# Performance work log

Measured on AMD Instinct MI355X. Metric: run time of the kernel, lower is better.

## Reference

```python
import jax, jax.numpy as jnp
import numpy as np
from jax import lax

NUM_CLASSES = 2
NUM_PROTO = 10
C = 720


def _conv(x, w, b, pad):
    # x: [B,Cin,H,W], w: [Cout,Cin,kh,kw]
    y = lax.conv_general_dilated(x, w, (1, 1), ((pad, pad), (pad, pad)),
                                 dimension_numbers=('NCHW', 'OIHW', 'NCHW'))
    return y + b[None, :, None, None]


def _bn(x, g, b, rm, rv):
    inv = g / jnp.sqrt(rv + 1e-5)
    return (x - rm[None, :, None, None]) * inv[None, :, None, None] + b[None, :, None, None]


def _ln(x, g, b):
    mu = jnp.mean(x, -1, keepdims=True)
    var = jnp.var(x, -1, keepdims=True)
    return (x - mu) / jnp.sqrt(var + 1e-5) * g + b


def _l2n(x):
    n = jnp.linalg.norm(x, axis=-1, keepdims=True)
    return x / jnp.maximum(n, 1e-12)


def _resize_bilinear_ac(x, oh, ow):
    # bilinear with align_corners=True, x: [B,C,H,W]
    B, Cc, H, W = x.shape
    ys = jnp.linspace(0.0, H - 1.0, oh)
    xs = jnp.linspace(0.0, W - 1.0, ow)
    y0 = jnp.floor(ys).astype(jnp.int32)
    y1 = jnp.minimum(y0 + 1, H - 1)
    wy = (ys - y0).astype(x.dtype)
    x0 = jnp.floor(xs).astype(jnp.int32)
    x1 = jnp.minimum(x0 + 1, W - 1)
    wx = (xs - x0).astype(x.dtype)
    r = x[:, :, y0, :] * (1 - wy)[None, None, :, None] + x[:, :, y1, :] * wy[None, None, :, None]
    return r[:, :, :, x0] * (1 - wx) + r[:, :, :, x1] * wx


def setup_inputs() -> dict:
    key = jax.random.key(0)
    ks = jax.random.split(key, 8)
    B, H = 2, 96
    f32 = jnp.float32
    return {
        'feat1': jax.random.normal(ks[0], (B, 48, H, H), f32),
        'feat2': jax.random.normal(ks[1], (B, 96, H // 2, H // 2), f32),
        'feat3': jax.random.normal(ks[2], (B, 192, H // 4, H // 4), f32),
        'feat4': jax.random.normal(ks[3], (B, 384, H // 8, H // 8), f32),
        'cls_w': jax.random.normal(ks[4], (C, C, 3, 3), f32) * 0.02,
        'cls_b': jnp.zeros((C,), f32),
        'cls_bn_g': jnp.ones((C,), f32),
        'cls_bn_b': jnp.zeros((C,), f32),
        'cls_bn_rm': jnp.zeros((C,), f32),
        'cls_bn_rv': jnp.ones((C,), f32),
        'proj_w1': jax.random.normal(ks[5], (C, C, 1, 1), f32) * 0.02,
        'proj_b1': jnp.zeros((C,), f32),
        'proj_bn_g': jnp.ones((C,), f32),
        'proj_bn_b': jnp.zeros((C,), f32),
        'proj_bn_rm': jnp.zeros((C,), f32),
        'proj_bn_rv': jnp.ones((C,), f32),
        'proj_w2': jax.random.normal(ks[6], (C, C, 1, 1), f32) * 0.02,
        'proj_b2': jnp.zeros((C,), f32),
        'ln_feat_g': jnp.ones((C,), f32),
        'ln_feat_b': jnp.zeros((C,), f32),
        'ln_mask_g': jnp.ones((NUM_CLASSES,), f32),
        'ln_mask_b': jnp.zeros((NUM_CLASSES,), f32),
        'prototypes': jax.random.normal(ks[7], (NUM_CLASSES, NUM_PROTO, C), f32) * 0.02,
    }


def reference(feat1, feat2, feat3, feat4, cls_w, cls_b, cls_bn_g, cls_bn_b, cls_bn_rm,
              cls_bn_rv, proj_w1, proj_b1, proj_bn_g, proj_bn_b, proj_bn_rm, proj_bn_rv,
              proj_w2, proj_b2, ln_feat_g, ln_feat_b, ln_mask_g, ln_mask_b, prototypes):
    B, _, h, w = feat1.shape
    feats = jnp.concatenate([
        feat1,
        _resize_bilinear_ac(feat2, h, w),
        _resize_bilinear_ac(feat3, h, w),
        _resize_bilinear_ac(feat4, h, w),
    ], axis=1)  # [B,720,h,w]
    # cls_head: Conv3x3 + BN + ReLU (Dropout2d is identity in eval)
    c = jax.nn.relu(_bn(_conv(feats, cls_w, cls_b, 1), cls_bn_g, cls_bn_b, cls_bn_rm, cls_bn_rv))
    # proj_head (convmlp): Conv1x1 + BN + ReLU + Conv1x1
    p = jax.nn.relu(_bn(_conv(c, proj_w1, proj_b1, 0), proj_bn_g, proj_bn_b, proj_bn_rm, proj_bn_rv))
    p = _conv(p, proj_w2, proj_b2, 0)
    # (b h w) c
    _c = p.transpose(0, 2, 3, 1).reshape(-1, C)
    _c = _l2n(_ln(_c, ln_feat_g, ln_feat_b))
    protos = _l2n(prototypes)  # [K,M,C]
    masks = jnp.einsum('nd,kmd->nmk', _c, protos)  # [N,M,K]
    out_seg = jnp.max(masks, axis=1)               # [N,K]
    out_seg = _ln(out_seg, ln_mask_g, ln_mask_b)
    out_seg = out_seg.reshape(B, h, w, NUM_CLASSES).transpose(0, 3, 1, 2)
    return out_seg
```

## Files before the change

### kernel.cpp

```cpp
#include <hip/hip_runtime.h>
#include <float.h>

#define WDIM 96
#define HW   9216
#define PH   98
#define IMG  (PH*PH)
#define NPIXP (2*IMG)
#define NPIX 19328
#define GUARD 128
#define GPIX (NPIX + 2*GUARD)
#define NKG_ACT 96
#define MDIM 768
#define G3 816
#define G1 96

typedef _Float16 f16;
typedef f16  f16x8 __attribute__((ext_vector_type(8)));
typedef f16  f16x4 __attribute__((ext_vector_type(4)));
typedef float f32x4 __attribute__((ext_vector_type(4)));

__global__ void prep_kernel(
    const float* __restrict__ cls_b,
    const float* __restrict__ g0, const float* __restrict__ b0,
    const float* __restrict__ rm0, const float* __restrict__ rv0,
    const float* __restrict__ p1b,
    const float* __restrict__ g1, const float* __restrict__ b1,
    const float* __restrict__ rm1, const float* __restrict__ rv1,
    const float* __restrict__ p2b,
    const float* __restrict__ protos,
    float* __restrict__ alpha, float* __restrict__ beta,
    float* __restrict__ protoN)
{
    __shared__ float red[4];
    if (blockIdx.x == 0) {
        for (int i = threadIdx.x; i < MDIM; i += blockDim.x) {
            if (i < 720) {
                float s0 = g0[i] * rsqrtf(rv0[i] + 1e-5f);
                alpha[i] = s0;
                beta[i]  = (cls_b[i] - rm0[i]) * s0 + b0[i];
                float s1 = g1[i] * rsqrtf(rv1[i] + 1e-5f);
                alpha[MDIM + i] = s1;
                beta[MDIM + i]  = (p1b[i] - rm1[i]) * s1 + b1[i];
                alpha[2*MDIM + i] = 1.0f;
                beta[2*MDIM + i]  = p2b[i];
            } else {
                alpha[i] = 0.f; beta[i] = 0.f;
                alpha[MDIM + i] = 0.f; beta[MDIM + i] = 0.f;
                alpha[2*MDIM + i] = 0.f; beta[2*MDIM + i] = 0.f;
            }
        }
    } else {
        int row = blockIdx.x - 1;
        const float* src = protos + row * 720;
        float s = 0.f;
        for (int i = threadIdx.x; i < 720; i += blockDim.x) { float v = src[i]; s += v * v; }
        #pragma unroll
        for (int off = 32; off > 0; off >>= 1) s += __shfl_down(s, off);
        int wave = threadIdx.x >> 6, lane = threadIdx.x & 63;
        if (lane == 0) red[wave] = s;
        __syncthreads();
        float tot = red[0] + red[1] + red[2] + red[3];
        float rn = 1.0f / fmaxf(sqrtf(tot), 1e-12f);
        for (int i = threadIdx.x; i < 720; i += blockDim.x)
            protoN[row * 720 + i] = src[i] * rn;
    }
}

__global__ __launch_bounds__(256)
void w3trans_kernel(const float* __restrict__ w3,
                    f16* __restrict__ W3h, f16* __restrict__ W3l)
{
    int tid = blockIdx.x * blockDim.x + threadIdx.x;
    int kgl = tid / MDIM;
    int o   = tid - kgl * MDIM;
    if (kgl > 90) return;

    if (kgl == 90) {
        f16x8 z = {0, 0, 0, 0, 0, 0, 0, 0};
        for (int g = 810; g < G3; ++g) {
            size_t off = ((size_t)g * MDIM + o) * 8;
            *(f16x8*)(W3h + off) = z;
            *(f16x8*)(W3l + off) = z;
        }
        return;
    }

    float buf[72];
    if (o < 720) {
        const float* src = w3 + (size_t)o * 6480 + kgl * 72;
        #pragma unroll
        for (int c = 0; c < 72; ++c) buf[c] = src[c];
    } else {
        #pragma unroll
        for (int c = 0; c < 72; ++c) buf[c] = 0.f;
    }

    #pragma unroll
    for (int s = 0; s < 9; ++s) {
        f16x8 hv, lv;
        #pragma unroll
        for (int c = 0; c < 8; ++c) {
            float v = buf[c * 9 + s];
            f16 h = (f16)v;
            hv[c] = h;
            lv[c] = (f16)(v - (float)h);
        }
        size_t off = ((size_t)(kgl * 9 + s) * MDIM + o) * 8;
        *(f16x8*)(W3h + off) = hv;
        *(f16x8*)(W3l + off) = lv;
    }
}

__global__ void w1trans_kernel(const float* __restrict__ w1a,
                               const float* __restrict__ w1b,
                               f16* __restrict__ W1ah, f16* __restrict__ W1al,
                               f16* __restrict__ W1bh, f16* __restrict__ W1bl)
{
    int tid = blockIdx.x * blockDim.x + threadIdx.x;
    const int N1 = G1 * MDIM;
    const float* src; f16 *dh, *dl; int g, o;
    if (tid < N1)            { g = tid / MDIM; o = tid - g * MDIM; src = w1a; dh = W1ah; dl = W1al; }
    else if (tid < 2 * N1)   { int u = tid - N1; g = u / MDIM; o = u - g * MDIM; src = w1b; dh = W1bh; dl = W1bl; }
    else return;

    float v[8];
    #pragma unroll
    for (int j = 0; j < 8; ++j) v[j] = 0.f;
    if (g < 90 && o < 720) {
        #pragma unroll
        for (int j = 0; j < 8; ++j)
            v[j] = src[(size_t)o * 720 + g * 8 + j];
    }
    f16x8 hv, lv;
    #pragma unroll
    for (int j = 0; j < 8; ++j) {
        f16 h = (f16)v[j];
        hv[j] = h;
        lv[j] = (f16)(v[j] - (float)h);
    }
    size_t off = ((size_t)g * MDIM + o) * 8;
    *(f16x8*)(dh + off) = hv;
    *(f16x8*)(dl + off) = lv;
}

__global__ void upsample_kernel(const float* __restrict__ f1,
                                const float* __restrict__ f2,
                                const float* __restrict__ f3,
                                const float* __restrict__ f4,
                                f16* __restrict__ Xhi, f16* __restrict__ Xlo)
{
    int tid = blockIdx.x * blockDim.x + threadIdx.x;
    if (tid >= 90 * GPIX) return;
    int kg = tid / GPIX;
    int gp = tid - kg * GPIX;
    int p  = gp - GUARD;
    float v[8];
    #pragma unroll
    for (int j = 0; j < 8; ++j) v[j] = 0.f;
    if (p >= 0 && p < NPIXP) {
        int b = p / IMG; int rem = p - b * IMG;
        int y = rem / PH; int x = rem - y * PH;
        if (y >= 1 && y <= 96 && x >= 1 && x <= 96) {
            int oy = y - 1, ox = x - 1;
            int c0 = kg * 8;
            if (c0 < 48) {
                #pragma unroll
                for (int j = 0; j < 8; ++j)
                    v[j] = f1[((size_t)(b * 48 + c0 + j)) * HW + oy * 96 + ox];
            } else {
                const float* src; int Cs, Hs, cb;
                if (c0 < 144)      { src = f2; Cs = 96;  Hs = 48; cb = c0 - 48; }
                else if (c0 < 336) { src = f3; Cs = 192; Hs = 24; cb = c0 - 144; }
                else               { src = f4; Cs = 384; Hs = 12; cb = c0 - 336; }
                float scale = (float)(Hs - 1) / 95.0f;
                float yf = oy * scale, xf = ox * scale;
                int y0 = (int)yf, x0 = (int)xf;
                float wy = yf - y0, wx = xf - x0;
                int y1 = min(y0 + 1, Hs - 1), x1 = min(x0 + 1, Hs - 1);
                #pragma unroll
                for (int j = 0; j < 8; ++j) {
                    const float* sb = src + (size_t)(b * Cs + cb + j) * Hs * Hs;
                    float v00 = sb[y0 * Hs + x0], v01 = sb[y0 * Hs + x1];
                    float v10 = sb[y1 * Hs + x0], v11 = sb[y1 * Hs + x1];
                    float r0 = v00 * (1.f - wy) + v10 * wy;
                    float r1 = v01 * (1.f - wy) + v11 * wy;
                    v[j] = r0 * (1.f - wx) + r1 * wx;
                }
            }
        }
    }
    f16x8 hv, lv;
    #pragma unroll
    for (int j = 0; j < 8; ++j) {
        f16 h = (f16)v[j];
        hv[j] = h;
        lv[j] = (f16)(v[j] - (float)h);
    }
    size_t off = (size_t)tid * 8;
    *(f16x8*)(Xhi + off) = hv;
    *(f16x8*)(Xlo + off) = lv;
}

template<int NSTEP, int CONV3>
__global__ __launch_bounds__(256, 2)
void mfma_gemm(const f16* __restrict__ Whi, const f16* __restrict__ Wlo,
               const f16* __restrict__ Bhi_, const f16* __restrict__ Blo_,
               f16* __restrict__ Ohi, f16* __restrict__ Olo,
               const float* __restrict__ alpha, const float* __restrict__ beta,
               int relu)
{
    const int l = blockIdx.x;
    const int xcd = l & 7;
    const int j0 = l >> 3;
    const int ncol = xcd * 19 + j0 / 6;
    if (ncol >= 151) return;
    const int m0 = (j0 % 6) * 128;
    const int n0 = ncol * 128;

    const int t = threadIdx.x;
    const int lane = t & 63, wid = t >> 6;
    const int wm = wid >> 1, wn = wid & 1;
    const int quad = lane >> 4, ln = lane & 15;

    f32x4 acc[4][4];
    #pragma unroll
    for (int i = 0; i < 4; ++i)
        #pragma unroll
        for (int j = 0; j < 4; ++j)
            acc[i][j] = (f32x4){0.f, 0.f, 0.f, 0.f};

    const int arow = m0 + wm * 64 + ln;
    const f16* Ah0 = Whi + ((size_t)quad * MDIM + arow) * 8;
    const f16* Al0 = Wlo + ((size_t)quad * MDIM + arow) * 8;
    const size_t astep = (size_t)4 * MDIM * 8;

    const int bcol = n0 + wn * 64 + ln;

    auto brow_of = [&](int step) -> long long {
        const int g = step * 4 + quad;
        if (CONV3) {
            int gc = min(g, 809);
            int kgl = gc / 9;
            int s = gc - kgl * 9;
            int d = (s / 3 - 1) * PH + (s % 3 - 1);
            return (long long)kgl * GPIX + d;
        }
        return (long long)min(g, G1 - 1) * GPIX;
    };

    auto load_b = [&](f16x8 (&dst)[8], int step) {
        const long long brow = brow_of(step);
        const f16* bh = Bhi_ + (brow + bcol) * 8;
        const f16* bl = Blo_ + (brow + bcol) * 8;
        #pragma unroll
        for (int nt = 0; nt < 4; ++nt) {
            dst[nt]     = *(const f16x8*)(bh + nt * 128);
            dst[nt + 4] = *(const f16x8*)(bl + nt * 128);
        }
    };
    auto load_a = [&](f16x8 (&dst)[8], int step) {
        const f16* Ah = Ah0 + (size_t)step * astep;
        const f16* Al = Al0 + (size_t)step * astep;
        #pragma unroll
        for (int mt = 0; mt < 4; ++mt) {
            dst[mt]     = *(const f16x8*)(Ah + mt * 128);
            dst[mt + 4] = *(const f16x8*)(Al + mt * 128);
        }
    };
    auto compute = [&](f16x8 (&av)[8], f16x8 (&bv)[8]) {
        #pragma unroll
        for (int mt = 0; mt < 4; ++mt)
            #pragma unroll
            for (int nt = 0; nt < 4; ++nt) {
                acc[mt][nt] = __builtin_amdgcn_mfma_f32_16x16x32_f16(av[mt],     bv[nt],     acc[mt][nt], 0, 0, 0);
                acc[mt][nt] = __builtin_amdgcn_mfma_f32_16x16x32_f16(av[mt],     bv[nt + 4], acc[mt][nt], 0, 0, 0);
                acc[mt][nt] = __builtin_amdgcn_mfma_f32_16x16x32_f16(av[mt + 4], bv[nt],     acc[mt][nt], 0, 0, 0);
            }
    };

    f16x8 aP[8], bP[8], aQ[8], bQ[8];

    load_a(aP, 0);
    load_b(bP, 0);

    int step = 0;
    #pragma unroll 1
    for (; step + 2 <= NSTEP; step += 2) {
        load_a(aQ, step + 1);
        load_b(bQ, step + 1);
        compute(aP, bP);
        load_a(aP, step + 2);
        load_b(bP, step + 2);
        compute(aQ, bQ);
    }
    if (step < NSTEP)
        compute(aP, bP);

    #pragma unroll
    for (int mt = 0; mt < 4; ++mt) {
        const int rowb = m0 + wm * 64 + mt * 16 + quad * 4;
        const float4 a4 = *(const float4*)(alpha + rowb);
        const float4 b4 = *(const float4*)(beta + rowb);
        const size_t kg = rowb >> 3;
        const int sub = rowb & 7;
        #pragma unroll
        for (int nt = 0; nt < 4; ++nt) {
            const int P = n0 + wn * 64 + nt * 16 + ln;
            float v0 = acc[mt][nt][0] * a4.x + b4.x;
            float v1 = acc[mt][nt][1] * a4.y + b4.y;
            float v2 = acc[mt][nt][2] * a4.z + b4.z;
            float v3 = acc[mt][nt][3] * a4.w + b4.w;
            if (relu) {
                v0 = fmaxf(v0, 0.f); v1 = fmaxf(v1, 0.f);
                v2 = fmaxf(v2, 0.f); v3 = fmaxf(v3, 0.f);
            }
            f16 h0 = (f16)v0, h1 = (f16)v1, h2 = (f16)v2, h3 = (f16)v3;
            f16x4 hv = {h0, h1, h2, h3};
            f16x4 lv = {(f16)(v0 - (float)h0), (f16)(v1 - (float)h1),
                        (f16)(v2 - (float)h2), (f16)(v3 - (float)h3)};
            size_t o = (kg * GPIX + P) * 8 + sub;
            *(f16x4*)(Ohi + o) = hv;
            *(f16x4*)(Olo + o) = lv;
        }
    }
}

__global__ __launch_bounds__(256)
void head_kernel(const f16* __restrict__ Yhi, const f16* __restrict__ Ylo,
                 const float* __restrict__ lng, const float* __restrict__ lnb,
                 const float* __restrict__ protoN,
                 const float* __restrict__ lmg, const float* __restrict__ lmb,
                 float* __restrict__ out)
{
    const int t = threadIdx.x;
    const int wv = t >> 6, lane = t & 63;
    const int pw = lane >> 4, sub = lane & 15;
    const int p = blockIdx.x * 16 + wv * 4 + pw;
    const int b = p / HW; const int r = p - b * HW;
    const int y = r / 96; const int x = r - y * 96;
    const size_t P = (size_t)b * IMG + (y + 1) * PH + (x + 1);

    f16x8 xh[6], xl[6];
    float s1 = 0.f, s2 = 0.f;
    #pragma unroll
    for (int k = 0; k < 6; ++k) {
        int kg = sub + 16 * k;
        if (kg < 90) {
            xh[k] = *(const f16x8*)(Yhi + ((size_t)kg * GPIX + P) * 8);
            xl[k] = *(const f16x8*)(Ylo + ((size_t)kg * GPIX + P) * 8);
            #pragma unroll
            for (int j = 0; j < 8; ++j) {
                float v = (float)xh[k][j] + (float)xl[k][j];
                s1 += v; s2 += v * v;
            }
        }
    }
    #pragma unroll
    for (int m = 1; m < 16; m <<= 1) {
        s1 += __shfl_xor(s1, m);
        s2 += __shfl_xor(s2, m);
    }
    float mu  = s1 * (1.0f / 720.0f);
    float var = s2 * (1.0f / 720.0f) - mu * mu;
    float inv = rsqrtf(var + 1e-5f);

    float dots[20];
    #pragma unroll
    for (int q = 0; q < 20; ++q) dots[q] = 0.f;
    float nrm = 0.f;
    #pragma unroll
    for (int k = 0; k < 6; ++k) {
        int kg = sub + 16 * k;
        if (kg < 90) {
            const int c0 = kg * 8;
            #pragma unroll
            for (int j = 0; j < 8; ++j) {
                const int c = c0 + j;
                float v = ((float)xh[k][j] + (float)xl[k][j] - mu) * inv * lng[c] + lnb[c];
                nrm += v * v;
                #pragma unroll
                for (int q = 0; q < 20; ++q)
                    dots[q] = fmaf(v, protoN[q * 720 + c], dots[q]);
            }
        }
    }
    #pragma unroll
    for (int m = 1; m < 16; m <<= 1) {
        nrm += __shfl_xor(nrm, m);
        #pragma unroll
        for (int q = 0; q < 20; ++q) dots[q] += __shfl_xor(dots[q], m);
    }

    if (sub == 0) {
        float rn = 1.0f / fmaxf(sqrtf(nrm), 1e-12f);
        float m0v = -FLT_MAX, m1v = -FLT_MAX;
        #pragma unroll
        for (int q = 0; q < 10; ++q) m0v = fmaxf(m0v, dots[q]);
        #pragma unroll
        for (int q = 10; q < 20; ++q) m1v = fmaxf(m1v, dots[q]);
        m0v *= rn; m1v *= rn;
        float mu2 = 0.5f * (m0v + m1v);
        float dv  = m0v - mu2;
        float va  = dv * dv;
        float iv  = rsqrtf(va + 1e-5f);
        float o0 = (m0v - mu2) * iv * lmg[0] + lmb[0];
        float o1 = (m1v - mu2) * iv * lmg[1] + lmb[1];
        out[b * (2 * HW) + r]      = o0;
        out[b * (2 * HW) + HW + r] = o1;
    }
}

extern "C" void kernel_launch(void* const* d_in, const int* in_sizes, int n_in,
                              void* d_out, int out_size, void* d_ws, size_t ws_size,
                              hipStream_t stream)
{
    const float* feat1      = (const float*)d_in[0];
    const float* feat2      = (const float*)d_in[1];
    const float* feat3      = (const float*)d_in[2];
    const float* feat4      = (const float*)d_in[3];
    const float* cls_w      = (const float*)d_in[4];
    const float* cls_b      = (const float*)d_in[5];
    const float* cls_bn_g   = (const float*)d_in[6];
    const float* cls_bn_b   = (const float*)d_in[7];
    const float* cls_bn_rm  = (const float*)d_in[8];
    const float* cls_bn_rv  = (const float*)d_in[9];
    const float* proj_w1    = (const float*)d_in[10];
    const float* proj_b1    = (const float*)d_in[11];
    const float* proj_bn_g  = (const float*)d_in[12];
    const float* proj_bn_b  = (const float*)d_in[13];
    const float* proj_bn_rm = (const float*)d_in[14];
    const float* proj_bn_rv = (const float*)d_in[15];
    const float* proj_w2    = (const float*)d_in[16];
    const float* proj_b2    = (const float*)d_in[17];
    const float* ln_feat_g  = (const float*)d_in[18];
    const float* ln_feat_b  = (const float*)d_in[19];
    const float* ln_mask_g  = (const float*)d_in[20];
    const float* ln_mask_b  = (const float*)d_in[21];
    const float* protos     = (const float*)d_in[22];

    const size_t PLANEH = (size_t)NKG_ACT * GPIX * 8;
    const size_t W3SZ   = (size_t)G3 * MDIM * 8;
    const size_t W1SZ   = (size_t)G1 * MDIM * 8;

    f16* Xhi  = (f16*)d_ws;
    f16* Xlo  = Xhi + PLANEH;
    f16* Yhi  = Xlo + PLANEH;
    f16* Ylo  = Yhi + PLANEH;
    f16* W3h  = Ylo + PLANEH;
    f16* W3l  = W3h + W3SZ;
    f16* W1ah = W3l + W3SZ;
    f16* W1al = W1ah + W1SZ;
    f16* W1bh = W1al + W1SZ;
    f16* W1bl = W1bh + W1SZ;
    float* alphas = (float*)(W1bl + W1SZ);
    float* betas  = alphas + 3 * MDIM;
    float* protoN = betas + 3 * MDIM;

    prep_kernel<<<21, 256, 0, stream>>>(cls_b, cls_bn_g, cls_bn_b, cls_bn_rm, cls_bn_rv,
                                        proj_b1, proj_bn_g, proj_bn_b, proj_bn_rm, proj_bn_rv,
                                        proj_b2, protos, alphas, betas, protoN);
    {
        int total = 91 * MDIM;
        w3trans_kernel<<<(total + 255) / 256, 256, 0, stream>>>(cls_w, W3h, W3l);
    }
    {
        int total = 2 * G1 * MDIM;
        w1trans_kernel<<<(total + 255) / 256, 256, 0, stream>>>(proj_w1, proj_w2,
                                                                W1ah, W1al, W1bh, W1bl);
    }
    {
        int total = 90 * GPIX;
        upsample_kernel<<<(total + 255) / 256, 256, 0, stream>>>(feat1, feat2, feat3, feat4,
                                                                 Xhi, Xlo);
    }

    const size_t GOFF = (size_t)GUARD * 8;
    const int NBLK = 912;
    mfma_gemm<203, 1><<<NBLK, 256, 0, stream>>>(W3h, W3l, Xhi + GOFF, Xlo + GOFF,
                                                Yhi + GOFF, Ylo + GOFF,
                                                alphas, betas, 1);
    mfma_gemm<23, 0><<<NBLK, 256, 0, stream>>>(W1ah, W1al, Yhi + GOFF, Ylo + GOFF,
                                               Xhi + GOFF, Xlo + GOFF,
                                               alphas + MDIM, betas + MDIM, 1);
    mfma_gemm<23, 0><<<NBLK, 256, 0, stream>>>(W1bh, W1bl, Xhi + GOFF, Xlo + GOFF,
                                               Yhi + GOFF, Ylo + GOFF,
                                               alphas + 2 * MDIM, betas + 2 * MDIM, 0);

    head_kernel<<<HW * 2 / 16, 256, 0, stream>>>(Yhi + GOFF, Ylo + GOFF,
                                                 ln_feat_g, ln_feat_b, protoN,
                                                 ln_mask_g, ln_mask_b, (float*)d_out);
}
```

Measured before the change: 857.3 us.

## Stage GEMM operand tiles through LDS with async global_load_lds double buffering

Replaces the per-wave direct global-to-register loads of A and B fragments with a double-buffered LDS staging scheme using global_load_lds. Each wave loads one K-group slice for the whole block, then all waves read their fragments from shared memory. This cuts redundant global loads, since each A/B row was previously fetched by two waves, and lets the copy engine fill LDS while the MFMAs run. The cost is a __syncthreads per step, extra LDS traffic and footprint that may reduce occupancy. There is also a risk that the final-iteration prefetch reads past the buffer bounds.

New measurement: 771.0 us. 10.1% less time.

```diff
diff --git a/kernel.cpp b/kernel.cpp
--- a/kernel.cpp
+++ b/kernel.cpp
@@ -18,6 +18,14 @@
 typedef f16  f16x8 __attribute__((ext_vector_type(8)));
 typedef f16  f16x4 __attribute__((ext_vector_type(4)));
 typedef float f32x4 __attribute__((ext_vector_type(4)));
+typedef unsigned int u32;
+
+typedef __attribute__((address_space(1))) const u32 gu32;
+typedef __attribute__((address_space(3))) u32 lu32;
+__device__ __forceinline__ void gld16(const f16* g, f16* s)
+{
+    __builtin_amdgcn_global_load_lds((gu32*)g, (lu32*)s, 16, 0, 0);
+}
 
 __global__ void prep_kernel(
     const float* __restrict__ cls_b,
@@ -209,6 +217,9 @@
                const float* __restrict__ alpha, const float* __restrict__ beta,
                int relu)
 {
+    __shared__ f16 sA[2][4][2][128][8];
+    __shared__ f16 sB[2][4][2][128][8];
+
     const int l = blockIdx.x;
     const int xcd = l & 7;
     const int j0 = l >> 3;
@@ -229,45 +240,54 @@
         for (int j = 0; j < 4; ++j)
             acc[i][j] = (f32x4){0.f, 0.f, 0.f, 0.f};
 
-    const int arow = m0 + wm * 64 + ln;
-    const f16* Ah0 = Whi + ((size_t)quad * MDIM + arow) * 8;
-    const f16* Al0 = Wlo + ((size_t)quad * MDIM + arow) * 8;
-    const size_t astep = (size_t)4 * MDIM * 8;
-
-    const int bcol = n0 + wn * 64 + ln;
-
-    auto brow_of = [&](int step) -> long long {
-        const int g = step * 4 + quad;
+    const f16* aH0 = Whi + ((size_t)wid * MDIM + m0 + lane) * 8;
+    const f16* aL0 = Wlo + ((size_t)wid * MDIM + m0 + lane) * 8;
+    const size_t aAdv = (size_t)4 * MDIM * 8;
+
+    auto stage = [&](int st, int b) {
+        const f16* ah = aH0 + (size_t)st * aAdv;
+        const f16* al = aL0 + (size_t)st * aAdv;
+        f16* dA = &sA[b][wid][0][0][0];
+        gld16(ah,       dA);
+        gld16(ah + 512, dA + 512);
+        gld16(al,       dA + 1024);
+        gld16(al + 512, dA + 1536);
+        const int g = 4 * st + wid;
+        long long brow;
         if (CONV3) {
-            int gc = min(g, 809);
+            int gc = g > 809 ? 809 : g;
             int kgl = gc / 9;
-            int s = gc - kgl * 9;
-            int d = (s / 3 - 1) * PH + (s % 3 - 1);
-            return (long long)kgl * GPIX + d;
-        }
-        return (long long)min(g, G1 - 1) * GPIX;
+            int s2 = gc - kgl * 9;
+            brow = (long long)kgl * GPIX + (s2 / 3 - 1) * PH + (s2 % 3 - 1);
+        } else {
+            int gc = g > G1 - 1 ? G1 - 1 : g;
+            brow = (long long)gc * GPIX;
+        }
+        const f16* bh = Bhi_ + (brow + n0 + lane) * 8;
+        const f16* bl = Blo_ + (brow + n0 + lane) * 8;
+        f16* dB = &sB[b][wid][0][0][0];
+        gld16(bh,       dB);
+        gld16(bh + 512, dB + 512);
+        gld16(bl,       dB + 1024);
+        gld16(bl + 512, dB + 1536);
     };
 
-    auto load_b = [&](f16x8 (&dst)[8], int step) {
-        const long long brow = brow_of(step);
-        const f16* bh = Bhi_ + (brow + bcol) * 8;
-        const f16* bl = Blo_ + (brow + bcol) * 8;
-        #pragma unroll
-        for (int nt = 0; nt < 4; ++nt) {
-            dst[nt]     = *(const f16x8*)(bh + nt * 128);
-            dst[nt + 4] = *(const f16x8*)(bl + nt * 128);
-        }
-    };
-    auto load_a = [&](f16x8 (&dst)[8], int step) {
-        const f16* Ah = Ah0 + (size_t)step * astep;
-        const f16* Al = Al0 + (size_t)step * astep;
+    stage(0, 0);
+    __syncthreads();
+
+    #pragma unroll 2
+    for (int s = 0; s < NSTEP; ++s) {
+        stage(s + 1, (s + 1) & 1);
+
+        const int cur = s & 1;
+        f16x8 av[8], bv[8];
         #pragma unroll
         for (int mt = 0; mt < 4; ++mt) {
-            dst[mt]     = *(const f16x8*)(Ah + mt * 128);
-            dst[mt + 4] = *(const f16x8*)(Al + mt * 128);
-        }
-    };
-    auto compute = [&](f16x8 (&av)[8], f16x8 (&bv)[8]) {
+            av[mt]     = *(const f16x8*)&sA[cur][quad][0][wm * 64 + mt * 16 + ln][0];
+            av[mt + 4] = *(const f16x8*)&sA[cur][quad][1][wm * 64 + mt * 16 + ln][0];
+            bv[mt]     = *(const f16x8*)&sB[cur][quad][0][wn * 64 + mt * 16 + ln][0];
+            bv[mt + 4] = *(const f16x8*)&sB[cur][quad][1][wn * 64 + mt * 16 + ln][0];
+        }
         #pragma unroll
         for (int mt = 0; mt < 4; ++mt)
             #pragma unroll
@@ -276,25 +296,9 @@
                 acc[mt][nt] = __builtin_amdgcn_mfma_f32_16x16x32_f16(av[mt],     bv[nt + 4], acc[mt][nt], 0, 0, 0);
                 acc[mt][nt] = __builtin_amdgcn_mfma_f32_16x16x32_f16(av[mt + 4], bv[nt],     acc[mt][nt], 0, 0, 0);
             }
-    };
-
-    f16x8 aP[8], bP[8], aQ[8], bQ[8];
-
-    load_a(aP, 0);
-    load_b(bP, 0);
-
-    int step = 0;
-    #pragma unroll 1
-    for (; step + 2 <= NSTEP; step += 2) {
-        load_a(aQ, step + 1);
-        load_b(bQ, step + 1);
-        compute(aP, bP);
-        load_a(aP, step + 2);
-        load_b(bP, step + 2);
-        compute(aQ, bQ);
-    }
-    if (step < NSTEP)
-        compute(aP, bP);
+
+        __syncthreads();
+    }
 
     #pragma unroll
     for (int mt = 0; mt < 4; ++mt) {
```
